# Kernel optimization log

Hardware: AMD Instinct MI355X
Metric: run time of the kernel (lower is better)

Reference implementation:

```python
import jax, jax.numpy as jnp
import numpy as np

DIM = 2048
NUM_HEADS = 16
HEAD_DIM = DIM // NUM_HEADS
HIDDEN = 4 * DIM
EPS = 1e-6


def rmsnorm(x, w):
    # Faithful to source: weight * (x * dim**-0.5 / sqrt(mean(x^2) + eps))
    scale = DIM ** -0.5
    norm = jnp.sqrt(jnp.mean(x * x, axis=-1, keepdims=True) + EPS)
    return w * (x * scale / norm)


def setup_inputs() -> dict:
    key = jax.random.key(0)
    ks = jax.random.split(key, 10)
    def init(k, shape, fan_in):
        return jax.random.normal(k, shape, dtype=jnp.float32) * (fan_in ** -0.5)
    return {
        "x": jax.random.normal(ks[0], (2, 2048, DIM), dtype=jnp.float32),
        "norm1_w": jnp.ones((DIM,), dtype=jnp.float32),
        "wq": init(ks[1], (DIM, DIM), DIM),
        "wk": init(ks[2], (HEAD_DIM, DIM), DIM),
        "wv": init(ks[3], (HEAD_DIM, DIM), DIM),
        "wo": init(ks[4], (DIM, DIM), DIM),
        "norm2_w": jnp.ones((DIM,), dtype=jnp.float32),
        "w1": init(ks[5], (HIDDEN, DIM), DIM),
        "w2": init(ks[6], (DIM, HIDDEN), HIDDEN),
        "w3": init(ks[7], (HIDDEN, DIM), DIM),
    }


def reference(x, norm1_w, wq, wk, wv, wo, norm2_w, w1, w2, w3):
    B, S, _ = x.shape
    # --- Multi-Query Attention (pre-norm) ---
    h = rmsnorm(x, norm1_w)
    q = h @ wq.T                                  # [B,S,D]
    k = h @ wk.T                                  # [B,S,hd] (shared across heads)
    v = h @ wv.T                                  # [B,S,hd]
    q = q.reshape(B, S, NUM_HEADS, HEAD_DIM)
    # scores: q @ k^T / sqrt(hd); k is broadcast (repeated) across heads
    scores = jnp.einsum('bshd,btd->bhst', q, k) / (HEAD_DIM ** 0.5)  # [B,H,S,S]
    probs = jax.nn.softmax(scores, axis=-1)
    attn = jnp.einsum('bhst,btd->bshd', probs, v).reshape(B, S, DIM)
    x = x + attn @ wo.T
    # --- SwiGLU FFN (pre-norm) ---
    h = rmsnorm(x, norm2_w)
    ffn = (jax.nn.silu(h @ w1.T) * (h @ w3.T)) @ w2.T
    return x + ffn
```

## Files before the change

kernel.cpp:

```cpp
#include <hip/hip_runtime.h>
#include <hip/hip_bf16.h>

typedef __attribute__((ext_vector_type(4))) float f32x4;
typedef __attribute__((ext_vector_type(8))) short s16x8;
typedef __attribute__((ext_vector_type(4))) short s16x4;
typedef __attribute__((ext_vector_type(2))) short s16x2;

#define MFMA_BF16 __builtin_amdgcn_mfma_f32_16x16x32_bf16

__device__ inline short f2bf(float f) {
  unsigned u = __float_as_uint(f);
  u = (u + 0x7FFFu + ((u >> 16) & 1u)) >> 16;
  return (short)u;
}
__device__ inline float bf2f(short s) {
  return __uint_as_float(((unsigned)(unsigned short)s) << 16);
}

#define DPPF(x, ctrl) __int_as_float(__builtin_amdgcn_update_dpp( \
    __float_as_int(x), __float_as_int(x), ctrl, 0xF, 0xF, false))
__device__ inline float rowmax16(float x) {
  x = fmaxf(x, DPPF(x, 0xB1));
  x = fmaxf(x, DPPF(x, 0x4E));
  x = fmaxf(x, DPPF(x, 0x124));
  x = fmaxf(x, DPPF(x, 0x128));
  return x;
}
__device__ inline float rowsum16(float x) {
  x += DPPF(x, 0xB1);
  x += DPPF(x, 0x4E);
  x += DPPF(x, 0x124);
  x += DPPF(x, 0x128);
  return x;
}

__global__ __launch_bounds__(256) void cvt_kernel(
    const float* __restrict__ in, short* __restrict__ out, int n, float scale)
{
  int idx = (blockIdx.x * 256 + threadIdx.x) * 8;
  if (idx >= n) return;
  f32x4 a = *(const f32x4*)(in + idx);
  f32x4 b = *(const f32x4*)(in + idx + 4);
  s16x8 o;
  #pragma unroll
  for (int j = 0; j < 4; ++j) { o[j] = f2bf(a[j] * scale); o[4 + j] = f2bf(b[j] * scale); }
  *(s16x8*)(out + idx) = o;
}

__global__ __launch_bounds__(256) void rmsnorm_kernel(
    const float* __restrict__ x, const float* __restrict__ w, short* __restrict__ out)
{
  size_t row = blockIdx.x;
  const float* xr = x + row * 2048;
  int base = threadIdx.x * 8;
  f32x4 a = *(const f32x4*)(xr + base);
  f32x4 b = *(const f32x4*)(xr + base + 4);
  float ss = a[0]*a[0] + a[1]*a[1] + a[2]*a[2] + a[3]*a[3]
           + b[0]*b[0] + b[1]*b[1] + b[2]*b[2] + b[3]*b[3];
  #pragma unroll
  for (int off = 1; off < 64; off <<= 1) ss += __shfl_xor(ss, off, 64);
  __shared__ float red[4];
  if ((threadIdx.x & 63) == 0) red[threadIdx.x >> 6] = ss;
  __syncthreads();
  float tot = red[0] + red[1] + red[2] + red[3];
  float rn = rsqrtf(tot * (1.0f / 2048.0f) + 1e-6f) * 0.022097086912079608f;
  f32x4 wa = *(const f32x4*)(w + base);
  f32x4 wb = *(const f32x4*)(w + base + 4);
  s16x8 o;
  #pragma unroll
  for (int j = 0; j < 4; ++j) {
    o[j]     = f2bf(a[j] * wa[j] * rn);
    o[4 + j] = f2bf(b[j] * wb[j] * rn);
  }
  *(s16x8*)(out + row * 2048 + base) = o;
}

template <int MODE>
__global__ __launch_bounds__(256, 2) void gemm_bt_kernel(
    const short* __restrict__ A, const short* __restrict__ B,
    void* __restrict__ Cv, const float* __restrict__ resid,
    int M, int N, int K)
{
  __shared__ short As[128 * 32];
  __shared__ short Bs[128 * 32];
  int tid = threadIdx.x;
  int lane = tid & 63;
  int w = tid >> 6;
  int r = lane & 15, g = lane >> 4;
  int wr = w >> 1, wc = w & 1;
  size_t row0 = (size_t)blockIdx.y * 128;
  size_t col0 = (size_t)blockIdx.x * 128;

  f32x4 acc[4][4];
  #pragma unroll
  for (int i = 0; i < 4; ++i)
    #pragma unroll
    for (int j = 0; j < 4; ++j) acc[i][j] = (f32x4){0.f, 0.f, 0.f, 0.f};

  const short* Ablk = A + row0 * K;
  const short* Bblk = B + col0 * K;
  int arow = tid >> 2;
  int akk = (tid & 3) << 3;

  for (int k0 = 0; k0 < K; k0 += 32) {
    #pragma unroll
    for (int i = 0; i < 2; ++i) {
      int chunk = i * 256 + tid;
      int rr = i * 64 + arow;
      __builtin_amdgcn_global_load_lds(
          (const __attribute__((address_space(1))) unsigned int*)(Ablk + (size_t)rr * K + k0 + akk),
          (__attribute__((address_space(3))) unsigned int*)(&As[chunk * 8]), 16, 0, 0);
      __builtin_amdgcn_global_load_lds(
          (const __attribute__((address_space(1))) unsigned int*)(Bblk + (size_t)rr * K + k0 + akk),
          (__attribute__((address_space(3))) unsigned int*)(&Bs[chunk * 8]), 16, 0, 0);
    }
    __syncthreads();
    s16x8 af[4], bfr[4];
    #pragma unroll
    for (int mm = 0; mm < 4; ++mm)
      af[mm] = *(const s16x8*)(&As[(wr * 64 + mm * 16 + r) * 32 + g * 8]);
    #pragma unroll
    for (int nn = 0; nn < 4; ++nn)
      bfr[nn] = *(const s16x8*)(&Bs[(wc * 64 + nn * 16 + r) * 32 + g * 8]);
    #pragma unroll
    for (int mm = 0; mm < 4; ++mm)
      #pragma unroll
      for (int nn = 0; nn < 4; ++nn)
        acc[mm][nn] = MFMA_BF16(af[mm], bfr[nn], acc[mm][nn], 0, 0, 0);
    __syncthreads();
  }

  #pragma unroll
  for (int mm = 0; mm < 4; ++mm) {
    #pragma unroll
    for (int nn = 0; nn < 4; ++nn) {
      #pragma unroll
      for (int j = 0; j < 4; ++j) {
        size_t rr = row0 + wr * 64 + mm * 16 + g * 4 + j;
        size_t cc = col0 + wc * 64 + nn * 16 + r;
        size_t idx = rr * (size_t)N + cc;
        if constexpr (MODE == 0) {
          ((short*)Cv)[idx] = f2bf(acc[mm][nn][j]);
        } else if constexpr (MODE == 1) {
          ((float*)Cv)[idx] = acc[mm][nn][j] + resid[idx];
        } else {
          short* gp = (short*)Cv;
          float gv = bf2f(gp[idx]);
          float sg = gv / (1.0f + __expf(-gv));
          gp[idx] = f2bf(sg * acc[mm][nn][j]);
        }
      }
    }
  }
}

__global__ __launch_bounds__(256) void transpose_v_kernel(
    const short* __restrict__ kv, short* __restrict__ vt)
{
  __shared__ short t[64][65];
  int b = blockIdx.z;
  int s0 = blockIdx.x * 64;
  int d0 = blockIdx.y * 64;
  int tid = threadIdx.x;
  #pragma unroll
  for (int i = 0; i < 16; ++i) {
    int e = i * 256 + tid;
    int sr = e >> 6, dc = e & 63;
    t[sr][dc] = kv[(size_t)(b * 2048 + s0 + sr) * 256 + 128 + d0 + dc];
  }
  __syncthreads();
  #pragma unroll
  for (int i = 0; i < 16; ++i) {
    int e = i * 256 + tid;
    int dr = e >> 6, sc = e & 63;
    vt[(size_t)b * 128 * 2048 + (size_t)(d0 + dr) * 2048 + s0 + sc] = t[sc][dr];
  }
}

__global__ __launch_bounds__(256, 2) void attn_kernel(
    const short* __restrict__ q, const short* __restrict__ kv,
    const short* __restrict__ vt, short* __restrict__ out)
{
  const int S = 2048;
  int tid = threadIdx.x;
  int w = tid >> 6;
  int lane = tid & 63;
  int r = lane & 15, g = lane >> 4;
  int h = blockIdx.y, b = blockIdx.z;
  int qrow0 = blockIdx.x * 128 + w * 32;

  __shared__ short Ks[2][4096];
  __shared__ short Vs[2][4096];
  __shared__ short Ps[4][32][40];

  const short* kvsrc = kv + (size_t)b * S * 256;
  const short* vsrc  = vt + (size_t)b * 128 * S;

  const short* qbase = q + ((size_t)(b * S + qrow0 + r)) * 2048 + h * 128;
  s16x8 qa[2][4];
  #pragma unroll
  for (int gq = 0; gq < 2; ++gq)
    #pragma unroll
    for (int dc = 0; dc < 4; ++dc)
      qa[gq][dc] = *(const s16x8*)(qbase + gq * 16 * 2048 + dc * 32 + g * 8);

  f32x4 o[2][8];
  #pragma unroll
  for (int gq = 0; gq < 2; ++gq)
    #pragma unroll
    for (int dt = 0; dt < 8; ++dt) o[gq][dt] = (f32x4){0.f, 0.f, 0.f, 0.f};
  float m[2][4], l[2][4];
  #pragma unroll
  for (int gq = 0; gq < 2; ++gq)
    #pragma unroll
    for (int j = 0; j < 4; ++j) { m[gq][j] = -1e30f; l[gq][j] = 0.f; }

#define STAGE(KVT, BSEL)                                                        \
  {                                                                             \
    int kv0s = (KVT) * 32;                                                      \
    _Pragma("unroll")                                                           \
    for (int i = 0; i < 2; ++i) {                                               \
      int c = w * 64 + lane + i * 256;                                          \
      int krow = c >> 4, kcp = c & 15;                                          \
      __builtin_amdgcn_global_load_lds(                                         \
          (const __attribute__((address_space(1))) unsigned int*)               \
              (kvsrc + (size_t)(kv0s + krow) * 256 + ((kcp ^ (krow & 7)) << 3)),\
          (__attribute__((address_space(3))) unsigned int*)(&Ks[BSEL][c * 8]),  \
          16, 0, 0);                                                            \
      int vrow = c >> 2, vcp = c & 3;                                           \
      __builtin_amdgcn_global_load_lds(                                         \
          (const __attribute__((address_space(1))) unsigned int*)               \
              (vsrc + (size_t)vrow * S + kv0s + ((vcp ^ (vrow & 3)) << 3)),     \
          (__attribute__((address_space(3))) unsigned int*)(&Vs[BSEL][c * 8]),  \
          16, 0, 0);                                                            \
    }                                                                           \
  }

  STAGE(0, 0);
  __syncthreads();

  for (int it = 0; it < 64; ++it) {
    int cur = it & 1;
    if (it < 63) STAGE(it + 1, cur ^ 1);

    s16x8 kc0[4], kc1[4], vb[8];
    #pragma unroll
    for (int dc = 0; dc < 4; ++dc) {
      kc0[dc] = *(const s16x8*)(&Ks[cur][r * 128 + (((dc * 4 + g) ^ (r & 7)) << 3)]);
      kc1[dc] = *(const s16x8*)(&Ks[cur][(16 + r) * 128 + (((dc * 4 + g) ^ (r & 7)) << 3)]);
    }
    #pragma unroll
    for (int dt = 0; dt < 8; ++dt)
      vb[dt] = *(const s16x8*)(&Vs[cur][(dt * 16 + r) * 32 + ((g ^ (r & 3)) << 3)]);

    f32x4 sc0[2], sc1[2];
    #pragma unroll
    for (int gq = 0; gq < 2; ++gq) { sc0[gq] = (f32x4){0.f,0.f,0.f,0.f}; sc1[gq] = (f32x4){0.f,0.f,0.f,0.f}; }
    __builtin_amdgcn_s_setprio(1);
    #pragma unroll
    for (int dc = 0; dc < 4; ++dc) {
      #pragma unroll
      for (int gq = 0; gq < 2; ++gq) {
        sc0[gq] = MFMA_BF16(qa[gq][dc], kc0[dc], sc0[gq], 0, 0, 0);
        sc1[gq] = MFMA_BF16(qa[gq][dc], kc1[dc], sc1[gq], 0, 0, 0);
      }
    }
    __builtin_amdgcn_s_setprio(0);

    float p0[2][4], p1[2][4];
    #pragma unroll
    for (int gq = 0; gq < 2; ++gq) {
      float mx[4];
      #pragma unroll
      for (int j = 0; j < 4; ++j) mx[j] = rowmax16(fmaxf(sc0[gq][j], sc1[gq][j]));
      bool nd = (mx[0] > m[gq][0] + 8.f) | (mx[1] > m[gq][1] + 8.f)
              | (mx[2] > m[gq][2] + 8.f) | (mx[3] > m[gq][3] + 8.f);
      if (__any(nd)) {
        #pragma unroll
        for (int j = 0; j < 4; ++j) {
          float mn = fmaxf(m[gq][j], mx[j]);
          float alpha = __expf(m[gq][j] - mn);
          m[gq][j] = mn;
          l[gq][j] *= alpha;
          #pragma unroll
          for (int dt = 0; dt < 8; ++dt) o[gq][dt][j] *= alpha;
        }
      }
      #pragma unroll
      for (int j = 0; j < 4; ++j) {
        p0[gq][j] = __expf(sc0[gq][j] - m[gq][j]);
        p1[gq][j] = __expf(sc1[gq][j] - m[gq][j]);
        l[gq][j] += p0[gq][j] + p1[gq][j];
      }
      #pragma unroll
      for (int j = 0; j < 4; ++j) {
        Ps[w][gq * 16 + g * 4 + j][r]      = f2bf(p0[gq][j]);
        Ps[w][gq * 16 + g * 4 + j][16 + r] = f2bf(p1[gq][j]);
      }
    }
    asm volatile("s_waitcnt lgkmcnt(0)" ::: "memory");
    __builtin_amdgcn_sched_barrier(0);
    s16x8 pa0 = *(const s16x8*)(&Ps[w][r][g * 8]);
    s16x8 pa1 = *(const s16x8*)(&Ps[w][16 + r][g * 8]);
    __builtin_amdgcn_s_setprio(1);
    #pragma unroll
    for (int dt = 0; dt < 8; ++dt) {
      o[0][dt] = MFMA_BF16(pa0, vb[dt], o[0][dt], 0, 0, 0);
      o[1][dt] = MFMA_BF16(pa1, vb[dt], o[1][dt], 0, 0, 0);
    }
    __builtin_amdgcn_s_setprio(0);
    __syncthreads();
  }

  #pragma unroll
  for (int gq = 0; gq < 2; ++gq) {
    float linv[4];
    #pragma unroll
    for (int j = 0; j < 4; ++j) linv[j] = 1.0f / rowsum16(l[gq][j]);
    short* ob = out + ((size_t)(b * S + qrow0 + gq * 16)) * 2048 + h * 128;
    #pragma unroll
    for (int dt = 0; dt < 8; ++dt)
      #pragma unroll
      for (int j = 0; j < 4; ++j)
        ob[(size_t)(g * 4 + j) * 2048 + dt * 16 + r] = f2bf(o[gq][dt][j] * linv[j]);
  }
#undef STAGE
}

extern "C" void kernel_launch(void* const* d_in, const int* in_sizes, int n_in,
                              void* d_out, int out_size, void* d_ws, size_t ws_size,
                              hipStream_t stream) {
  const float* x   = (const float*)d_in[0];
  const float* n1w = (const float*)d_in[1];
  const float* wq  = (const float*)d_in[2];
  const float* wk  = (const float*)d_in[3];
  const float* wv  = (const float*)d_in[4];
  const float* wo  = (const float*)d_in[5];
  const float* n2w = (const float*)d_in[6];
  const float* w1  = (const float*)d_in[7];
  const float* w2  = (const float*)d_in[8];
  const float* w3  = (const float*)d_in[9];
  float* out = (float*)d_out;
  char* ws = (char*)d_ws;
  const size_t MB = 1ull << 20;
  short* wqb  = (short*)(ws);
  short* wob  = (short*)(ws + 8 * MB);
  short* w1b  = (short*)(ws + 16 * MB);
  short* w2b  = (short*)(ws + 48 * MB);
  short* w3b  = (short*)(ws + 80 * MB);
  short* wkvb = (short*)(ws + 112 * MB);
  short* h1   = (short*)(ws + 113 * MB);
  short* gbuf = (short*)(ws + 129 * MB);
  short* qb   = (short*)(ws + 129 * MB);
  short* kvb  = (short*)(ws + 145 * MB);
  short* vtb  = (short*)(ws + 147 * MB);

  const float qscale = 0.08838834764831845f;
  cvt_kernel<<<2048, 256, 0, stream>>>(wq, wqb, 4194304, qscale);
  cvt_kernel<<<128,  256, 0, stream>>>(wk, wkvb, 262144, 1.0f);
  cvt_kernel<<<128,  256, 0, stream>>>(wv, wkvb + 262144, 262144, 1.0f);
  cvt_kernel<<<2048, 256, 0, stream>>>(wo, wob, 4194304, 1.0f);
  cvt_kernel<<<8192, 256, 0, stream>>>(w1, w1b, 16777216, 1.0f);
  cvt_kernel<<<8192, 256, 0, stream>>>(w2, w2b, 16777216, 1.0f);
  cvt_kernel<<<8192, 256, 0, stream>>>(w3, w3b, 16777216, 1.0f);

  rmsnorm_kernel<<<4096, 256, 0, stream>>>(x, n1w, h1);
  gemm_bt_kernel<0><<<dim3(16, 32), 256, 0, stream>>>(h1, wqb, qb, nullptr, 4096, 2048, 2048);
  gemm_bt_kernel<0><<<dim3(2, 32), 256, 0, stream>>>(h1, wkvb, kvb, nullptr, 4096, 256, 2048);
  transpose_v_kernel<<<dim3(32, 2, 2), 256, 0, stream>>>(kvb, vtb);
  attn_kernel<<<dim3(16, 16, 2), 256, 0, stream>>>(qb, kvb, vtb, h1);
  gemm_bt_kernel<1><<<dim3(16, 32), 256, 0, stream>>>(h1, wob, out, x, 4096, 2048, 2048);
  rmsnorm_kernel<<<4096, 256, 0, stream>>>(out, n2w, h1);
  gemm_bt_kernel<0><<<dim3(64, 32), 256, 0, stream>>>(h1, w1b, gbuf, nullptr, 4096, 8192, 2048);
  gemm_bt_kernel<2><<<dim3(64, 32), 256, 0, stream>>>(h1, w3b, gbuf, nullptr, 4096, 8192, 2048);
  gemm_bt_kernel<1><<<dim3(16, 32), 256, 0, stream>>>(gbuf, w2b, out, out, 4096, 2048, 8192);
}
```

Before: 921.9 us.

## Replace GEMMs with 8-wave 256-row tile kernel using direct-to-LDS pipelined loads

Adds a new 512-thread GEMM kernel with 256xBN tiles. Global tiles are copied straight into swizzled LDS with global_load_lds and double-buffered, so loads for the next k-step overlap with MFMA work. It also interleaves the MFMA phases with barriers and priority hints, and remaps workgroups for L2 locality. All large projections (q, o, w1, w3, w2) switch to this kernel to raise MFMA utilisation. The cost is heavy register and LDS use, which can limit occupancy, plus reliance on hand-tuned vmcnt waits.

```diff
diff --git a/kernel.cpp b/kernel.cpp
--- a/kernel.cpp
+++ b/kernel.cpp
@@ -148,6 +148,159 @@
           float gv = bf2f(gp[idx]);
           float sg = gv / (1.0f + __expf(-gv));
           gp[idx] = f2bf(sg * acc[mm][nn][j]);
+        }
+      }
+    }
+  }
+}
+
+
+#define STAGEA(T, KH)                                                          \
+  _Pragma("unroll")                                                            \
+  for (int i = 0; i < 2; ++i) {                                                \
+    int lc = i * 512 + tid;                                                    \
+    int rw = lc >> 2, cp = lc & 3;                                             \
+    __builtin_amdgcn_global_load_lds(                                          \
+        (const __attribute__((address_space(1))) unsigned int*)                \
+            (Ablk + (size_t)rw * K + (T) * 64 + (KH) * 32 +                    \
+             ((cp ^ ((rw >> 1) & 3)) << 3)),                                   \
+        (__attribute__((address_space(3))) unsigned int*)                      \
+            (&As[(T) & 1][KH][lc * 8]), 16, 0, 0);                             \
+  }
+
+#define STAGEB(T, KH)                                                          \
+  _Pragma("unroll")                                                            \
+  for (int i = 0; i < BLOADS; ++i) {                                           \
+    int lc = i * 512 + tid;                                                    \
+    int rw = lc >> 2, cp = lc & 3;                                             \
+    __builtin_amdgcn_global_load_lds(                                          \
+        (const __attribute__((address_space(1))) unsigned int*)                \
+            (Bblk + (size_t)rw * K + (T) * 64 + (KH) * 32 +                    \
+             ((cp ^ ((rw >> 1) & 3)) << 3)),                                   \
+        (__attribute__((address_space(3))) unsigned int*)                      \
+            (&Bs[(T) & 1][KH][lc * 8]), 16, 0, 0);                             \
+  }
+
+#define LDA8(D, KH, MH)                                                        \
+  _Pragma("unroll")                                                            \
+  for (int mi = 0; mi < 4; ++mi) {                                             \
+    int rowa = wr * 128 + ((MH) * 4 + mi) * 16 + r;                            \
+    a[mi] = *(const s16x8*)(&As[D][KH][rowa * 32 + chsw * 8]);                 \
+  }
+
+#define LDB8(D, KH)                                                            \
+  _Pragma("unroll")                                                            \
+  for (int ni = 0; ni < NREP; ++ni) {                                          \
+    int rowb = wc * WN + ni * 16 + r;                                          \
+    b[ni] = *(const s16x8*)(&Bs[D][KH][rowb * 32 + chsw * 8]);                 \
+  }
+
+#define MF16(MH)                                                               \
+  __builtin_amdgcn_s_setprio(1);                                               \
+  _Pragma("unroll")                                                            \
+  for (int mi = 0; mi < 4; ++mi)                                               \
+    _Pragma("unroll")                                                          \
+    for (int ni = 0; ni < NREP; ++ni)                                          \
+      acc[(MH) * 4 + mi][ni] =                                                 \
+          MFMA_BF16(a[mi], b[ni], acc[(MH) * 4 + mi][ni], 0, 0, 0);            \
+  __builtin_amdgcn_s_setprio(0);
+
+#define WAITC                                                                  \
+  do {                                                                         \
+    if constexpr (BN == 256)                                                   \
+      asm volatile("s_waitcnt vmcnt(4)" ::: "memory");                         \
+    else                                                                       \
+      asm volatile("s_waitcnt vmcnt(3)" ::: "memory");                         \
+  } while (0)
+
+#define BAR __builtin_amdgcn_s_barrier()
+
+template <int BN, int MODE>
+__global__ __launch_bounds__(512, 2) void gemm8p_kernel(
+    const short* __restrict__ A, const short* __restrict__ B,
+    void* __restrict__ Cv, const float* __restrict__ resid,
+    int M, int N, int K)
+{
+  constexpr int BLOADS = BN / 128;
+  constexpr int WN = BN / 4;
+  constexpr int NREP = WN / 16;
+  __shared__ short As[2][2][256 * 32];
+  __shared__ short Bs[2][2][BN * 32];
+
+  int tid = threadIdx.x;
+  int lane = tid & 63;
+  int w = tid >> 6;
+  int r = lane & 15, g = lane >> 4;
+  int wr = w >> 2, wc = w & 3;
+  int chsw = g ^ ((r >> 1) & 3);
+
+  int nwg = gridDim.x * gridDim.y;
+  int orig = blockIdx.y * gridDim.x + blockIdx.x;
+  int swz = (orig & 7) * (nwg >> 3) + (orig >> 3);
+  int bx = swz % gridDim.x, by = swz / gridDim.x;
+  size_t row0 = (size_t)by * 256;
+  size_t col0 = (size_t)bx * BN;
+
+  const short* Ablk = A + row0 * K;
+  const short* Bblk = B + col0 * K;
+
+  f32x4 acc[8][NREP];
+  #pragma unroll
+  for (int i = 0; i < 8; ++i)
+    #pragma unroll
+    for (int j = 0; j < NREP; ++j) acc[i][j] = (f32x4){0.f, 0.f, 0.f, 0.f};
+
+  s16x8 a[4], b[NREP];
+  int NT = K >> 6;
+
+  STAGEA(0, 0); STAGEB(0, 0); STAGEA(0, 1); STAGEB(0, 1);
+  WAITC;
+  BAR;
+
+  for (int t = 0; t < NT; ++t) {
+    int d = t & 1;
+    bool nl = (t < NT - 1);
+    LDA8(d, 0, 0); LDB8(d, 0);
+    if (nl) { STAGEA(t + 1, 0); }
+    BAR;
+    MF16(0);
+    BAR;
+    LDA8(d, 0, 1);
+    if (nl) { STAGEB(t + 1, 0); WAITC; }
+    else    { asm volatile("s_waitcnt vmcnt(0)" ::: "memory"); }
+    BAR;
+    MF16(1);
+    BAR;
+    LDA8(d, 1, 0); LDB8(d, 1);
+    if (nl) { STAGEA(t + 1, 1); }
+    BAR;
+    MF16(0);
+    BAR;
+    LDA8(d, 1, 1);
+    if (nl) { STAGEB(t + 1, 1); WAITC; }
+    BAR;
+    MF16(1);
+    BAR;
+  }
+
+  #pragma unroll
+  for (int mi = 0; mi < 8; ++mi) {
+    #pragma unroll
+    for (int ni = 0; ni < NREP; ++ni) {
+      #pragma unroll
+      for (int j = 0; j < 4; ++j) {
+        size_t rr = row0 + wr * 128 + mi * 16 + g * 4 + j;
+        size_t cc = col0 + wc * WN + ni * 16 + r;
+        size_t idx = rr * (size_t)N + cc;
+        if constexpr (MODE == 0) {
+          ((short*)Cv)[idx] = f2bf(acc[mi][ni][j]);
+        } else if constexpr (MODE == 1) {
+          ((float*)Cv)[idx] = acc[mi][ni][j] + resid[idx];
+        } else {
+          short* gp = (short*)Cv;
+          float gv = bf2f(gp[idx]);
+          float sg = gv / (1.0f + __expf(-gv));
+          gp[idx] = f2bf(sg * acc[mi][ni][j]);
         }
       }
     }
@@ -365,13 +518,13 @@
   cvt_kernel<<<8192, 256, 0, stream>>>(w3, w3b, 16777216, 1.0f);
 
   rmsnorm_kernel<<<4096, 256, 0, stream>>>(x, n1w, h1);
-  gemm_bt_kernel<0><<<dim3(16, 32), 256, 0, stream>>>(h1, wqb, qb, nullptr, 4096, 2048, 2048);
+  gemm8p_kernel<128, 0><<<dim3(16, 16), 512, 0, stream>>>(h1, wqb, qb, nullptr, 4096, 2048, 2048);
   gemm_bt_kernel<0><<<dim3(2, 32), 256, 0, stream>>>(h1, wkvb, kvb, nullptr, 4096, 256, 2048);
   transpose_v_kernel<<<dim3(32, 2, 2), 256, 0, stream>>>(kvb, vtb);
   attn_kernel<<<dim3(16, 16, 2), 256, 0, stream>>>(qb, kvb, vtb, h1);
-  gemm_bt_kernel<1><<<dim3(16, 32), 256, 0, stream>>>(h1, wob, out, x, 4096, 2048, 2048);
+  gemm8p_kernel<128, 1><<<dim3(16, 16), 512, 0, stream>>>(h1, wob, out, x, 4096, 2048, 2048);
   rmsnorm_kernel<<<4096, 256, 0, stream>>>(out, n2w, h1);
-  gemm_bt_kernel<0><<<dim3(64, 32), 256, 0, stream>>>(h1, w1b, gbuf, nullptr, 4096, 8192, 2048);
-  gemm_bt_kernel<2><<<dim3(64, 32), 256, 0, stream>>>(h1, w3b, gbuf, nullptr, 4096, 8192, 2048);
-  gemm_bt_kernel<1><<<dim3(16, 32), 256, 0, stream>>>(gbuf, w2b, out, out, 4096, 2048, 8192);
-}
+  gemm8p_kernel<256, 0><<<dim3(32, 16), 512, 0, stream>>>(h1, w1b, gbuf, nullptr, 4096, 8192, 2048);
+  gemm8p_kernel<256, 2><<<dim3(32, 16), 512, 0, stream>>>(h1, w3b, gbuf, nullptr, 4096, 8192, 2048);
+  gemm8p_kernel<128, 1><<<dim3(16, 16), 512, 0, stream>>>(gbuf, w2b, out, out, 4096, 2048, 8192);
+}
```

Result: faster. 897.6 us (-2.6%).
